# Kernel optimization log

Measured on AMD Instinct MI355X. Metric: run time of the kernel, lower is better.

The kernel has to match this reference:

```python
import jax, jax.numpy as jnp
import numpy as np

B, S, D, DFF = 4, 2048, 1024, 4096
EPS = 1e-5


def layernorm(x, gamma, beta):
    mu = jnp.mean(x, axis=-1, keepdims=True)
    var = jnp.var(x, axis=-1, keepdims=True)
    return (x - mu) * jax.lax.rsqrt(var + EPS) * gamma + beta


def attention(Q, K, V, causal):
    d_k = Q.shape[-1]
    scores = jnp.einsum('bqd,bkd->bqk', Q, K) / jnp.sqrt(jnp.asarray(d_k, Q.dtype))
    if causal:
        q_len, k_len = scores.shape[-2], scores.shape[-1]
        mask = jnp.tril(jnp.ones((q_len, k_len), dtype=bool))
        scores = jnp.where(mask[None], scores, jnp.asarray(-jnp.inf, scores.dtype))
    w = jax.nn.softmax(scores, axis=-1)
    return jnp.einsum('bqk,bkd->bqd', w, V)


def setup_inputs() -> dict:
    key = jax.random.key(0)
    ks = jax.random.split(key, 12)
    sd = 0.02
    return {
        'y': jax.random.normal(ks[0], (B, S, D), jnp.float32),
        'Z': jax.random.normal(ks[1], (B, S, D), jnp.float32),
        'w1': jax.random.normal(ks[2], (D, DFF), jnp.float32) * sd,
        'b1': jnp.zeros((DFF,), jnp.float32),
        'w2': jax.random.normal(ks[3], (DFF, D), jnp.float32) * sd,
        'b2': jnp.zeros((D,), jnp.float32),
        'g1': jnp.ones((D,), jnp.float32), 'beta1': jnp.zeros((D,), jnp.float32),
        'g2': jnp.ones((D,), jnp.float32), 'beta2': jnp.zeros((D,), jnp.float32),
        'g3': jnp.ones((D,), jnp.float32), 'beta3': jnp.zeros((D,), jnp.float32),
    }


def reference(y, Z, w1, b1, w2, b2, g1, beta1, g2, beta2, g3, beta3):
    # masked (causal) self-attention, single head over full d_model
    sa = attention(y, y, y, causal=True)
    y = layernorm(y + sa, g1, beta1)
    # cross-attention to encoder memory Z
    ca = attention(y, Z, Z, causal=False)
    y = layernorm(y + ca, g2, beta2)
    # position-wise FFN
    h = jax.nn.relu(jnp.einsum('bsd,df->bsf', y, w1) + b1)
    ff = jnp.einsum('bsf,fd->bsd', h, w2) + b2
    y = layernorm(y + ff, g3, beta3)
    return y
```

## Files before the change

kernel.cpp:

```cpp
#include <hip/hip_runtime.h>
#include <hip/hip_bf16.h>


#define Bb 4
#define Ss 2048
#define Dd 1024
#define Ff 4096

typedef __attribute__((ext_vector_type(4))) float f32x4;
typedef __attribute__((ext_vector_type(8))) short bf16x8;
typedef __attribute__((ext_vector_type(8))) unsigned short u16x8;
typedef __attribute__((ext_vector_type(4))) unsigned short u16x4;

__device__ __forceinline__ unsigned short f2bf(float f) {
  unsigned u = __float_as_uint(f);
  u += 0x7FFFu + ((u >> 16) & 1u);
  return (unsigned short)(u >> 16);
}
__device__ __forceinline__ float bf2f(unsigned short h) {
  return __uint_as_float(((unsigned)h) << 16);
}

__device__ __forceinline__ void gload_lds16(const void* g, void* l) {
  __builtin_amdgcn_global_load_lds((const __attribute__((address_space(1))) void*)g,
                                   (__attribute__((address_space(3))) void*)l, 16, 0, 0);
}

__device__ __forceinline__ int xcd8(int orig, int n) {
  int q = n >> 3, r = n & 7;
  int x = orig & 7;
  int base = x < r ? x * (q + 1) : r * (q + 1) + (x - r) * q;
  return base + (orig >> 3);
}

__global__ __launch_bounds__(256) void k_transpose_cast(const float* __restrict__ in,
                                                        unsigned short* __restrict__ outT,
                                                        unsigned short* __restrict__ outR,
                                                        int R, int C) {
  __shared__ float t[32][33];
  size_t bo = (size_t)blockIdx.z * R * C;
  const float* pin = in + bo;
  unsigned short* poutT = outT + bo;
  unsigned short* poutR = outR ? outR + bo : nullptr;
  int c0 = blockIdx.x * 32, r0 = blockIdx.y * 32;
  int tx = threadIdx.x, ty = threadIdx.y;
#pragma unroll
  for (int i = 0; i < 4; i++) {
    float v = pin[(size_t)(r0 + ty + i * 8) * C + c0 + tx];
    t[ty + i * 8][tx] = v;
    if (poutR) poutR[(size_t)(r0 + ty + i * 8) * C + c0 + tx] = f2bf(v);
  }
  __syncthreads();
#pragma unroll
  for (int i = 0; i < 4; i++)
    poutT[(size_t)(c0 + ty + i * 8) * R + r0 + tx] = f2bf(t[tx][ty + i * 8]);
}

#define BAR() __builtin_amdgcn_s_barrier()
#define PRIO1() __builtin_amdgcn_s_setprio(1)
#define PRIO0() __builtin_amdgcn_s_setprio(0)

#define LDA8(arr, mh, bo)                                                       \
  {                                                                             \
    _Pragma("unroll") for (int j_ = 0; j_ < QM; ++j_) {                         \
      _Pragma("unroll") for (int kh_ = 0; kh_ < 2; ++kh_) {                     \
        arr[j_][kh_] =                                                          \
            *(const bf16x8*)(lds + (bo) + ((mh)*QM + j_) * 2048 + aof[kh_]);    \
      }                                                                         \
    }                                                                           \
  }

#define LDB8(arr, nh, bo)                                                       \
  {                                                                             \
    _Pragma("unroll") for (int n_ = 0; n_ < 2; ++n_) {                          \
      _Pragma("unroll") for (int kh_ = 0; kh_ < 2; ++kh_) {                     \
        arr[n_][kh_] =                                                          \
            *(const bf16x8*)(lds + (bo) + ((nh)*2 + n_) * 2048 + bof[kh_]);     \
      }                                                                         \
    }                                                                           \
  }

#define MMQ(aarr, barr, mh, nh)                                                 \
  {                                                                             \
    _Pragma("unroll") for (int j_ = 0; j_ < QM; ++j_) {                         \
      _Pragma("unroll") for (int n_ = 0; n_ < 2; ++n_) {                        \
        _Pragma("unroll") for (int kh_ = 0; kh_ < 2; ++kh_) {                   \
          acc[(mh)*QM + j_][(nh)*2 + n_] = __builtin_amdgcn_mfma_f32_16x16x32_bf16( \
              aarr[j_][kh_], barr[n_][kh_], acc[(mh)*QM + j_][(nh)*2 + n_], 0, 0, 0); \
        }                                                                       \
      }                                                                         \
    }                                                                           \
  }

#define EPILOGUE(MR_, WMS_)                                                     \
  {                                                                             \
    const int colb = j0 + wc * 64 + fr;                                         \
    const int rowb = i0 + wr * (WMS_) + (kq << 2);                              \
    const size_t cb = (size_t)bz * bsC;                                         \
    _Pragma("unroll") for (int m = 0; m < (MR_); ++m) {                         \
      _Pragma("unroll") for (int r = 0; r < 4; ++r) {                           \
        size_t ro = cb + (size_t)(rowb + m * 16 + r) * ldc;                     \
        _Pragma("unroll") for (int n = 0; n < 4; ++n) {                         \
          float v = acc[m][n][r];                                               \
          int col = colb + n * 16;                                              \
          if (EPI == 0) Cb[ro + col] = f2bf(v * scale);                         \
          else if (EPI == 2) Cb[ro + col] = f2bf(fmaxf(v + bias[col], 0.f));    \
          else if (EPI == 4) Cb[ro + col] = f2bf(v + resid[ro + col]);          \
          else Cb[ro + col] = f2bf(v + bias[col] + resid[ro + col]);            \
        }                                                                       \
      }                                                                         \
    }                                                                           \
  }

template <int EPI, bool CAUSAL>
__global__ __launch_bounds__(512) void k_gemm8(
    const unsigned short* __restrict__ Ag, const unsigned short* __restrict__ Bg,
    unsigned short* __restrict__ Cb,
    const float* __restrict__ bias, const float* __restrict__ resid,
    int K, int lda, int ldb, int ldc, long bsA, long bsB, long bsC, float scale) {
  constexpr int QM = 4;
  constexpr int ABYTES = 32768, BBYTES = 32768;
  __shared__ alignas(16) char lds[2 * ABYTES + 2 * BBYTES];

  int i0, j0;
  if (CAUSAL) {
    int t = xcd8(blockIdx.x, gridDim.x);
    int ti = (int)((sqrtf(8.f * t + 1.f) - 1.f) * 0.5f);
    while ((ti + 1) * (ti + 2) / 2 <= t) ++ti;
    while (ti * (ti + 1) / 2 > t) --ti;
    i0 = ti * 256;
    j0 = (t - ti * (ti + 1) / 2) * 256;
  } else {
    int lin = xcd8(blockIdx.y * gridDim.x + blockIdx.x, gridDim.x * gridDim.y);
    i0 = (lin / gridDim.x) * 256;
    j0 = (lin % gridDim.x) * 256;
  }
  int bz = blockIdx.z;
  Ag += (size_t)bz * bsA;
  Bg += (size_t)bz * bsB;

  const int nk = K / 64;
  const int niter = nk / 2;

  const int tid = threadIdx.x;
  const int w = tid >> 6, lane = tid & 63;
  const int wr = w >> 2, wc = w & 3;

  const int srow = (w << 3) + (lane >> 3);
  const int bcs = (lane & 7) ^ (lane >> 3);
  const unsigned short* As = Ag + (size_t)(i0 + srow) * lda + bcs * 8;
  const unsigned short* Bs = Bg + (size_t)(j0 + srow) * ldb + bcs * 8;
  char* ldsAw = lds + w * 1024;
  char* ldsBw = lds + 2 * ABYTES + w * 1024;

  auto stA = [&](int kt, int hf) {
    int ks = kt < nk ? kt : nk - 1;
#pragma unroll
    for (int l = 0; l < 2; ++l)
      gload_lds16(As + (size_t)(hf * 128 + l * 64) * lda + ks * 64,
                  ldsAw + (kt & 1) * ABYTES + hf * 128 * 128 + l * 8192);
  };
  auto stB = [&](int kt, int hf) {
    int ks = kt < nk ? kt : nk - 1;
#pragma unroll
    for (int l = 0; l < 2; ++l)
      gload_lds16(Bs + (size_t)(hf * 128 + l * 64) * ldb + ks * 64,
                  ldsBw + (kt & 1) * BBYTES + hf * 128 * 128 + l * 8192);
  };

  const int fr = lane & 15, kq = lane >> 4;
  const int rA = wr * 128 + fr;
  const int rB = wc * 64 + fr;
  unsigned aof[2], bof[2];
  aof[0] = rA * 128 + ((kq ^ (rA & 7)) << 4);
  aof[1] = rA * 128 + (((kq + 4) ^ (rA & 7)) << 4);
  bof[0] = 2 * ABYTES + rB * 128 + ((kq ^ (rB & 7)) << 4);
  bof[1] = 2 * ABYTES + rB * 128 + (((kq + 4) ^ (rB & 7)) << 4);
  constexpr int A0 = 0, A1 = ABYTES, B0 = 0, B1 = BBYTES;

  f32x4 acc[8][4];
#pragma unroll
  for (int m = 0; m < 8; ++m)
#pragma unroll
    for (int n = 0; n < 4; ++n) acc[m][n] = (f32x4){0.f, 0.f, 0.f, 0.f};

  bf16x8 a0[QM][2], a1[QM][2], b0[2][2], b1[2][2];

  stA(0, 0); stA(0, 1); stB(0, 0); stB(0, 1);
  stA(1, 0); stA(1, 1); stB(1, 0);
  asm volatile("s_waitcnt vmcnt(6)" ::: "memory");
  BAR();
  LDA8(a0, 0, A0); LDB8(b0, 0, B0);

  for (int t = 0; t < niter; ++t) {
    const int ka = 2 * t + 2, kb = 2 * t + 3;
    LDA8(a1, 1, A0);
    stB(2 * t + 1, 1);
    BAR(); PRIO1(); MMQ(a0, b0, 0, 0); PRIO0(); BAR();
    LDB8(b1, 1, B0);
    stA(ka, 0);
    BAR(); PRIO1(); MMQ(a1, b0, 1, 0); PRIO0(); BAR();
    stA(ka, 1);
    BAR(); PRIO1(); MMQ(a0, b1, 0, 1); PRIO0(); BAR();
    stB(ka, 0);
    asm volatile("s_waitcnt vmcnt(6)" ::: "memory");
    BAR();
    LDA8(a0, 0, A1); LDB8(b0, 0, B1);
    PRIO1(); MMQ(a1, b1, 1, 1); PRIO0(); BAR();
    LDA8(a1, 1, A1);
    stB(ka, 1);
    BAR(); PRIO1(); MMQ(a0, b0, 0, 0); PRIO0(); BAR();
    LDB8(b1, 1, B1);
    stA(kb, 0);
    BAR(); PRIO1(); MMQ(a1, b0, 1, 0); PRIO0(); BAR();
    stA(kb, 1);
    BAR(); PRIO1(); MMQ(a0, b1, 0, 1); PRIO0(); BAR();
    stB(kb, 0);
    asm volatile("s_waitcnt vmcnt(6)" ::: "memory");
    BAR();
    LDA8(a0, 0, A0); LDB8(b0, 0, B0);
    PRIO1(); MMQ(a1, b1, 1, 1); PRIO0(); BAR();
  }
  EPILOGUE(8, 128)
}

template <int EPI, bool KCAP>
__global__ __launch_bounds__(512) void k_gemm4(
    const unsigned short* __restrict__ Ag, const unsigned short* __restrict__ Bg,
    unsigned short* __restrict__ Cb,
    const float* __restrict__ bias, const float* __restrict__ resid,
    int K, int lda, int ldb, int ldc, long bsA, long bsB, long bsC, float scale) {
  constexpr int QM = 4;
  constexpr int ABYTES = 16384, BBYTES = 32768;
  __shared__ alignas(16) char lds[2 * ABYTES + 2 * BBYTES];

  int lin = xcd8(blockIdx.y * gridDim.x + blockIdx.x, gridDim.x * gridDim.y);
  int i0 = (lin / gridDim.x) * 128;
  int j0 = (lin % gridDim.x) * 256;
  int bz = blockIdx.z;
  Ag += (size_t)bz * bsA;
  Bg += (size_t)bz * bsB;

  int nk = K / 64;
  if (KCAP) {
    int cap = i0 / 64 + 2;
    nk = nk < cap ? nk : cap;
  }
  const int niter = nk / 2;

  const int tid = threadIdx.x;
  const int w = tid >> 6, lane = tid & 63;
  const int wr = w >> 2, wc = w & 3;

  const int srow = (w << 3) + (lane >> 3);
  const int bcs = (lane & 7) ^ (lane >> 3);
  const unsigned short* As = Ag + (size_t)(i0 + srow) * lda + bcs * 8;
  const unsigned short* Bs = Bg + (size_t)(j0 + srow) * ldb + bcs * 8;
  char* ldsAw = lds + w * 1024;
  char* ldsBw = lds + 2 * ABYTES + w * 1024;

  auto stA2 = [&](int kt) {
    int ks = kt < nk ? kt : nk - 1;
#pragma unroll
    for (int hf = 0; hf < 2; ++hf)
      gload_lds16(As + (size_t)(hf * 64) * lda + ks * 64,
                  ldsAw + (kt & 1) * ABYTES + hf * 64 * 128);
  };
  auto stBh = [&](int kt, int hf) {
    int ks = kt < nk ? kt : nk - 1;
#pragma unroll
    for (int l = 0; l < 2; ++l)
      gload_lds16(Bs + (size_t)(hf * 128 + l * 64) * ldb + ks * 64,
                  ldsBw + (kt & 1) * BBYTES + hf * 128 * 128 + l * 8192);
  };

  const int fr = lane & 15, kq = lane >> 4;
  const int rA = wr * 64 + fr;
  const int rB = wc * 64 + fr;
  unsigned aof[2], bof[2];
  aof[0] = rA * 128 + ((kq ^ (rA & 7)) << 4);
  aof[1] = rA * 128 + (((kq + 4) ^ (rA & 7)) << 4);
  bof[0] = 2 * ABYTES + rB * 128 + ((kq ^ (rB & 7)) << 4);
  bof[1] = 2 * ABYTES + rB * 128 + (((kq + 4) ^ (rB & 7)) << 4);
  constexpr int A0 = 0, A1 = ABYTES, B0 = 0, B1 = BBYTES;

  f32x4 acc[4][4];
#pragma unroll
  for (int m = 0; m < 4; ++m)
#pragma unroll
    for (int n = 0; n < 4; ++n) acc[m][n] = (f32x4){0.f, 0.f, 0.f, 0.f};

  bf16x8 a[QM][2], b0[2][2], b1[2][2];

  stA2(0); stBh(0, 0); stBh(0, 1);
  stA2(1); stBh(1, 0);
  asm volatile("s_waitcnt vmcnt(4)" ::: "memory");
  BAR();
  LDA8(a, 0, A0); LDB8(b0, 0, B0);

  for (int t = 0; t < niter; ++t) {
    const int ka = 2 * t + 2, kb = 2 * t + 3;
    LDB8(b1, 1, B0);
    stBh(2 * t + 1, 1);
    BAR(); PRIO1(); MMQ(a, b0, 0, 0); PRIO0(); BAR();
    stA2(ka); stBh(ka, 0);
    asm volatile("s_waitcnt vmcnt(4)" ::: "memory");
    BAR();
    PRIO1(); MMQ(a, b1, 0, 1); PRIO0();
    LDA8(a, 0, A1); LDB8(b0, 0, B1);
    BAR();
    LDB8(b1, 1, B1);
    stBh(ka, 1);
    BAR(); PRIO1(); MMQ(a, b0, 0, 0); PRIO0(); BAR();
    stA2(kb); stBh(kb, 0);
    asm volatile("s_waitcnt vmcnt(4)" ::: "memory");
    BAR();
    PRIO1(); MMQ(a, b1, 0, 1); PRIO0();
    LDA8(a, 0, A0); LDB8(b0, 0, B0);
    BAR();
  }
  EPILOGUE(4, 64)
}

template <bool CAUSAL>
__global__ __launch_bounds__(256) void k_softmax(unsigned short* __restrict__ scores) {
  int row = blockIdx.x;
  int i = row & (Ss - 1);
  unsigned short* src = scores + (size_t)row * Ss;
  int nv = CAUSAL ? i + 1 : Ss;
  int nb = CAUSAL ? ((i & ~127) + 128) : Ss;
  int t = threadIdx.x;
  int w = t >> 6, lane = t & 63;
  bool act = t * 8 < nb;
  float v[8];
  float mx = -1e30f;
  if (act) {
    u16x8 raw = *(const u16x8*)(src + t * 8);
#pragma unroll
    for (int k = 0; k < 8; k++) {
      int j = t * 8 + k;
      v[k] = (j < nv) ? bf2f(raw[k]) : -1e30f;
      mx = fmaxf(mx, v[k]);
    }
  } else {
#pragma unroll
    for (int k = 0; k < 8; k++) v[k] = -1e30f;
  }
#pragma unroll
  for (int o = 32; o; o >>= 1) mx = fmaxf(mx, __shfl_xor(mx, o));
  __shared__ float red[8];
  if (lane == 0) red[w] = mx;
  __syncthreads();
  mx = fmaxf(fmaxf(red[0], red[1]), fmaxf(red[2], red[3]));
  float sum = 0.f;
#pragma unroll
  for (int k = 0; k < 8; k++) {
    float e = (v[k] > -1e29f) ? __expf(v[k] - mx) : 0.f;
    v[k] = e;
    sum += e;
  }
#pragma unroll
  for (int o = 32; o; o >>= 1) sum += __shfl_xor(sum, o);
  if (lane == 0) red[4 + w] = sum;
  __syncthreads();
  sum = red[4] + red[5] + red[6] + red[7];
  float inv = 1.f / sum;
  if (act) {
    u16x8 r;
#pragma unroll
    for (int k = 0; k < 8; k++) r[k] = f2bf(v[k] * inv);
    *(u16x8*)(src + t * 8) = r;
  }
}

__global__ __launch_bounds__(256) void k_ln(const unsigned short* __restrict__ a,
                                            const float* __restrict__ g,
                                            const float* __restrict__ be,
                                            float* __restrict__ outf,
                                            unsigned short* __restrict__ outb) {
  int row = blockIdx.x;
  size_t o = (size_t)row * Dd;
  int t = threadIdx.x;
  u16x4 raw = *(const u16x4*)(a + o + t * 4);
  f32x4 x;
#pragma unroll
  for (int k = 0; k < 4; k++) x[k] = bf2f(raw[k]);
  float s = x[0] + x[1] + x[2] + x[3];
  float q = x[0] * x[0] + x[1] * x[1] + x[2] * x[2] + x[3] * x[3];
  int w = t >> 6, lane = t & 63;
#pragma unroll
  for (int of = 32; of; of >>= 1) {
    s += __shfl_xor(s, of);
    q += __shfl_xor(q, of);
  }
  __shared__ float red[8];
  if (lane == 0) {
    red[w] = s;
    red[4 + w] = q;
  }
  __syncthreads();
  s = red[0] + red[1] + red[2] + red[3];
  q = red[4] + red[5] + red[6] + red[7];
  float mean = s * (1.f / Dd);
  float var = q * (1.f / Dd) - mean * mean;
  float rstd = rsqrtf(var + 1e-5f);
  f32x4 gv = *(const f32x4*)(g + t * 4);
  f32x4 bv = *(const f32x4*)(be + t * 4);
  f32x4 y;
#pragma unroll
  for (int k = 0; k < 4; k++) y[k] = (x[k] - mean) * rstd * gv[k] + bv[k];
  *(f32x4*)(outf + o + t * 4) = y;
  if (outb) {
    u16x4 r;
    r[0] = f2bf(y[0]); r[1] = f2bf(y[1]); r[2] = f2bf(y[2]); r[3] = f2bf(y[3]);
    *(u16x4*)(outb + o + t * 4) = r;
  }
}

extern "C" void kernel_launch(void* const* d_in, const int* in_sizes, int n_in, void* d_out,
                              int out_size, void* d_ws, size_t ws_size, hipStream_t stream) {
  (void)in_sizes; (void)n_in; (void)out_size; (void)ws_size;
  const float* y   = (const float*)d_in[0];
  const float* Z   = (const float*)d_in[1];
  const float* w1  = (const float*)d_in[2];
  const float* b1  = (const float*)d_in[3];
  const float* w2  = (const float*)d_in[4];
  const float* b2  = (const float*)d_in[5];
  const float* g1  = (const float*)d_in[6];
  const float* be1 = (const float*)d_in[7];
  const float* g2  = (const float*)d_in[8];
  const float* be2 = (const float*)d_in[9];
  const float* g3  = (const float*)d_in[10];
  const float* be3 = (const float*)d_in[11];
  float* out = (float*)d_out;

  char* ws = (char*)d_ws;
  const size_t MB = 1024ull * 1024ull;
  unsigned short* T   = (unsigned short*)(ws);
  unsigned short* Zbf = (unsigned short*)(ws + 16 * MB);
  unsigned short* ybf = (unsigned short*)(ws + 32 * MB);
  unsigned short* w1t = (unsigned short*)(ws + 48 * MB);
  unsigned short* w2t = (unsigned short*)(ws + 56 * MB);
  unsigned short* sc  = (unsigned short*)(ws + 64 * MB);
  unsigned short* h   = (unsigned short*)(ws + 64 * MB);
  unsigned short* Zt  = (unsigned short*)(ws + 96 * MB);
  float* res          = (float*)(ws + 128 * MB);
  unsigned short* attnb = (unsigned short*)d_out;

  dim3 b256(256), b512(512);
  const float scl = 1.f / 32.f;
  const long SD = (long)Ss * Dd, SS = (long)Ss * Ss;

  k_transpose_cast<<<dim3(Dd / 32, Ss / 32, Bb), dim3(32, 8), 0, stream>>>(y, T, ybf, Ss, Dd);
  k_transpose_cast<<<dim3(Dd / 32, Ss / 32, Bb), dim3(32, 8), 0, stream>>>(Z, Zt, Zbf, Ss, Dd);
  k_transpose_cast<<<dim3(Ff / 32, Dd / 32, 1), dim3(32, 8), 0, stream>>>(w1, w1t, nullptr, Dd, Ff);
  k_transpose_cast<<<dim3(Dd / 32, Ff / 32, 1), dim3(32, 8), 0, stream>>>(w2, w2t, nullptr, Ff, Dd);

  k_gemm8<0, true><<<dim3(36, 1, Bb), b512, 0, stream>>>(
      ybf, ybf, sc, nullptr, nullptr, Dd, Dd, Dd, Ss, SD, SD, SS, scl);
  k_softmax<true><<<dim3(Bb * Ss), b256, 0, stream>>>(sc);
  k_gemm4<4, true><<<dim3(Dd / 256, Ss / 128, Bb), b512, 0, stream>>>(
      sc, T, attnb, nullptr, y, Ss, Ss, Ss, Dd, SS, SD, SD, 1.f);
  k_ln<<<dim3(Bb * Ss), b256, 0, stream>>>(attnb, g1, be1, res, ybf);

  k_gemm8<0, false><<<dim3(Ss / 256, Ss / 256, Bb), b512, 0, stream>>>(
      ybf, Zbf, sc, nullptr, nullptr, Dd, Dd, Dd, Ss, SD, SD, SS, scl);
  k_softmax<false><<<dim3(Bb * Ss), b256, 0, stream>>>(sc);
  k_gemm4<4, false><<<dim3(Dd / 256, Ss / 128, Bb), b512, 0, stream>>>(
      sc, Zt, attnb, nullptr, res, Ss, Ss, Ss, Dd, SS, SD, SD, 1.f);
  k_ln<<<dim3(Bb * Ss), b256, 0, stream>>>(attnb, g2, be2, res, ybf);

  k_gemm8<2, false><<<dim3(Ff / 256, (Bb * Ss) / 256, 1), b512, 0, stream>>>(
      ybf, w1t, h, b1, nullptr, Dd, Dd, Dd, Ff, 0L, 0L, 0L, 1.f);
  k_gemm4<5, false><<<dim3(Dd / 256, (Bb * Ss) / 128, 1), b512, 0, stream>>>(
      h, w2t, T, b2, res, Ff, Ff, Ff, Dd, 0L, 0L, 0L, 1.f);
  k_ln<<<dim3(Bb * Ss), b256, 0, stream>>>(T, g3, be3, out, nullptr);
}
```

Measured before the change: 376.3 us.

## Compute attention score GEMMs in FP8 e4m3 with permuted-column layout

The two QK^T score GEMMs (causal self-attention and cross-attention) now run on FP8 e4m3 MFMA instead of bf16. Their inputs (y, Z and the first LayerNorm output) are emitted as FP8 with a per-64-byte column permutation so the new kernel's LDS reads line up with the fp8 MFMA operand layout. This halves the input bytes and LDS footprint for those GEMMs and uses the faster fp8 matrix instructions. The cost is reduced precision in the attention scores: unnormalized inputs of magnitude up to about 4 with K=1024 could push softmax errors past tolerance.

```diff
diff --git a/kernel.cpp b/kernel.cpp
--- a/kernel.cpp
+++ b/kernel.cpp
@@ -1,5 +1,6 @@
 #include <hip/hip_runtime.h>
 #include <hip/hip_bf16.h>
+#include <hip/hip_fp8.h>
 
 
 #define Bb 4
@@ -9,6 +10,7 @@
 
 typedef __attribute__((ext_vector_type(4))) float f32x4;
 typedef __attribute__((ext_vector_type(8))) short bf16x8;
+typedef __attribute__((ext_vector_type(2))) long i64x2;
 typedef __attribute__((ext_vector_type(8))) unsigned short u16x8;
 typedef __attribute__((ext_vector_type(4))) unsigned short u16x4;
 
@@ -19,6 +21,14 @@
 }
 __device__ __forceinline__ float bf2f(unsigned short h) {
   return __uint_as_float(((unsigned)h) << 16);
+}
+__device__ __forceinline__ unsigned char f2f8(float f) {
+  __hip_fp8_e4m3 q(f);
+  return q.__x;
+}
+__device__ __forceinline__ int f8col(int c) {
+  int g = c >> 6, b = c & 63, o = b >> 3, j = b & 7;
+  return g * 64 + (2 * (o & 3) + (o >> 2)) * 8 + j;
 }
 
 __device__ __forceinline__ void gload_lds16(const void* g, void* l) {
@@ -35,20 +45,20 @@
 
 __global__ __launch_bounds__(256) void k_transpose_cast(const float* __restrict__ in,
                                                         unsigned short* __restrict__ outT,
-                                                        unsigned short* __restrict__ outR,
+                                                        unsigned char* __restrict__ out8,
                                                         int R, int C) {
   __shared__ float t[32][33];
   size_t bo = (size_t)blockIdx.z * R * C;
   const float* pin = in + bo;
   unsigned short* poutT = outT + bo;
-  unsigned short* poutR = outR ? outR + bo : nullptr;
+  unsigned char* pout8 = out8 ? out8 + bo : nullptr;
   int c0 = blockIdx.x * 32, r0 = blockIdx.y * 32;
   int tx = threadIdx.x, ty = threadIdx.y;
 #pragma unroll
   for (int i = 0; i < 4; i++) {
     float v = pin[(size_t)(r0 + ty + i * 8) * C + c0 + tx];
     t[ty + i * 8][tx] = v;
-    if (poutR) poutR[(size_t)(r0 + ty + i * 8) * C + c0 + tx] = f2bf(v);
+    if (pout8) pout8[(size_t)(r0 + ty + i * 8) * C + f8col(c0 + tx)] = f2f8(v);
   }
   __syncthreads();
 #pragma unroll
@@ -87,6 +97,28 @@
         _Pragma("unroll") for (int kh_ = 0; kh_ < 2; ++kh_) {                   \
           acc[(mh)*QM + j_][(nh)*2 + n_] = __builtin_amdgcn_mfma_f32_16x16x32_bf16( \
               aarr[j_][kh_], barr[n_][kh_], acc[(mh)*QM + j_][(nh)*2 + n_], 0, 0, 0); \
+        }                                                                       \
+      }                                                                         \
+    }                                                                           \
+  }
+
+#define LDAF8(arr, mh, bo)                                                      \
+  {                                                                             \
+    _Pragma("unroll") for (int j_ = 0; j_ < 4; ++j_)                            \
+        arr[j_] = *(const i64x2*)(lds + (bo) + ((mh)*4 + j_) * 1024 + aofs);    \
+  }
+#define LDBF8(arr, nh, bo)                                                      \
+  {                                                                             \
+    _Pragma("unroll") for (int n_ = 0; n_ < 2; ++n_)                            \
+        arr[n_] = *(const i64x2*)(lds + (bo) + ((nh)*2 + n_) * 1024 + bofs);    \
+  }
+#define MMQF8(aarr, barr, mh, nh)                                               \
+  {                                                                             \
+    _Pragma("unroll") for (int j_ = 0; j_ < 4; ++j_) {                          \
+      _Pragma("unroll") for (int n_ = 0; n_ < 2; ++n_) {                        \
+        _Pragma("unroll") for (int kh_ = 0; kh_ < 2; ++kh_) {                   \
+          acc[(mh)*4 + j_][(nh)*2 + n_] = __builtin_amdgcn_mfma_f32_16x16x32_fp8_fp8( \
+              aarr[j_][kh_], barr[n_][kh_], acc[(mh)*4 + j_][(nh)*2 + n_], 0, 0, 0);  \
         }                                                                       \
       }                                                                         \
     }                                                                           \
@@ -112,6 +144,120 @@
     }                                                                           \
   }
 
+template <bool CAUSAL>
+__global__ __launch_bounds__(512) void k_gemm8f8(
+    const unsigned char* __restrict__ Ag, const unsigned char* __restrict__ Bg,
+    unsigned short* __restrict__ Cb,
+    int K, int lda, int ldb, int ldc, long bsA, long bsB, long bsC, float scale) {
+  constexpr int ABYTES = 16384, BBYTES = 16384;
+  __shared__ alignas(16) char lds[2 * ABYTES + 2 * BBYTES];
+
+  int i0, j0;
+  if (CAUSAL) {
+    int t = xcd8(blockIdx.x, gridDim.x);
+    int ti = (int)((sqrtf(8.f * t + 1.f) - 1.f) * 0.5f);
+    while ((ti + 1) * (ti + 2) / 2 <= t) ++ti;
+    while (ti * (ti + 1) / 2 > t) --ti;
+    i0 = ti * 256;
+    j0 = (t - ti * (ti + 1) / 2) * 256;
+  } else {
+    int lin = xcd8(blockIdx.y * gridDim.x + blockIdx.x, gridDim.x * gridDim.y);
+    i0 = (lin / gridDim.x) * 256;
+    j0 = (lin % gridDim.x) * 256;
+  }
+  int bz = blockIdx.z;
+  Ag += (size_t)bz * bsA;
+  Bg += (size_t)bz * bsB;
+
+  const int nk = K / 64;
+  const int niter = nk / 2;
+
+  const int tid = threadIdx.x;
+  const int w = tid >> 6, lane = tid & 63;
+  const int wr = w >> 2, wc = w & 3;
+
+  const int srow = tid >> 2;
+  const int scs = (tid & 3) ^ ((tid >> 3) & 3);
+  const unsigned char* As = Ag + (size_t)(i0 + srow) * lda + scs * 16;
+  const unsigned char* Bs = Bg + (size_t)(j0 + srow) * ldb + scs * 16;
+
+  auto stA = [&](int kt, int hf) {
+    int ks = kt < nk ? kt : nk - 1;
+    gload_lds16(As + (size_t)(hf * 128) * lda + ks * 64,
+                lds + (kt & 1) * ABYTES + hf * 8192 + w * 1024);
+  };
+  auto stB = [&](int kt, int hf) {
+    int ks = kt < nk ? kt : nk - 1;
+    gload_lds16(Bs + (size_t)(hf * 128) * ldb + ks * 64,
+                lds + 2 * ABYTES + (kt & 1) * BBYTES + hf * 8192 + w * 1024);
+  };
+
+  const int fr = lane & 15, kq = lane >> 4;
+  const int rA = wr * 128 + fr;
+  const int rB = wc * 64 + fr;
+  const unsigned aofs = rA * 64 + ((kq ^ ((rA >> 1) & 3)) << 4);
+  const unsigned bofs = rB * 64 + ((kq ^ ((rB >> 1) & 3)) << 4);
+  constexpr int A0 = 0, A1 = ABYTES, B0 = 2 * ABYTES, B1 = 2 * ABYTES + BBYTES;
+
+  f32x4 acc[8][4];
+#pragma unroll
+  for (int m = 0; m < 8; ++m)
+#pragma unroll
+    for (int n = 0; n < 4; ++n) acc[m][n] = (f32x4){0.f, 0.f, 0.f, 0.f};
+
+  i64x2 a0[4], a1[4], b0[2], b1[2];
+
+  stA(0, 0); stA(0, 1); stB(0, 0); stB(0, 1);
+  stA(1, 0); stA(1, 1); stB(1, 0);
+  asm volatile("s_waitcnt vmcnt(3)" ::: "memory");
+  BAR();
+  LDAF8(a0, 0, A0); LDBF8(b0, 0, B0);
+
+  for (int t = 0; t < niter; ++t) {
+    const int ka = 2 * t + 2, kb = 2 * t + 3;
+    LDAF8(a1, 1, A0);
+    stB(2 * t + 1, 1);
+    BAR(); PRIO1(); MMQF8(a0, b0, 0, 0); PRIO0(); BAR();
+    LDBF8(b1, 1, B0);
+    stA(ka, 0);
+    BAR(); PRIO1(); MMQF8(a1, b0, 1, 0); PRIO0(); BAR();
+    stA(ka, 1);
+    BAR(); PRIO1(); MMQF8(a0, b1, 0, 1); PRIO0(); BAR();
+    stB(ka, 0);
+    asm volatile("s_waitcnt vmcnt(3)" ::: "memory");
+    BAR();
+    LDAF8(a0, 0, A1); LDBF8(b0, 0, B1);
+    PRIO1(); MMQF8(a1, b1, 1, 1); PRIO0(); BAR();
+    LDAF8(a1, 1, A1);
+    stB(ka, 1);
+    BAR(); PRIO1(); MMQF8(a0, b0, 0, 0); PRIO0(); BAR();
+    LDBF8(b1, 1, B1);
+    stA(kb, 0);
+    BAR(); PRIO1(); MMQF8(a1, b0, 1, 0); PRIO0(); BAR();
+    stA(kb, 1);
+    BAR(); PRIO1(); MMQF8(a0, b1, 0, 1); PRIO0(); BAR();
+    stB(kb, 0);
+    asm volatile("s_waitcnt vmcnt(3)" ::: "memory");
+    BAR();
+    LDAF8(a0, 0, A0); LDBF8(b0, 0, B0);
+    PRIO1(); MMQF8(a1, b1, 1, 1); PRIO0(); BAR();
+  }
+
+  const int colb = j0 + wc * 64 + fr;
+  const int rowb = i0 + wr * 128 + (kq << 2);
+  const size_t cb = (size_t)bz * bsC;
+#pragma unroll
+  for (int m = 0; m < 8; ++m) {
+#pragma unroll
+    for (int r = 0; r < 4; ++r) {
+      size_t ro = cb + (size_t)(rowb + m * 16 + r) * ldc;
+#pragma unroll
+      for (int n = 0; n < 4; ++n)
+        Cb[ro + colb + n * 16] = f2bf(acc[m][n][r] * scale);
+    }
+  }
+}
+
 template <int EPI, bool CAUSAL>
 __global__ __launch_bounds__(512) void k_gemm8(
     const unsigned short* __restrict__ Ag, const unsigned short* __restrict__ Bg,
@@ -373,11 +519,13 @@
   }
 }
 
+template <int OM>
 __global__ __launch_bounds__(256) void k_ln(const unsigned short* __restrict__ a,
                                             const float* __restrict__ g,
                                             const float* __restrict__ be,
                                             float* __restrict__ outf,
-                                            unsigned short* __restrict__ outb) {
+                                            unsigned short* __restrict__ outb,
+                                            unsigned char* __restrict__ out8) {
   int row = blockIdx.x;
   size_t o = (size_t)row * Dd;
   int t = threadIdx.x;
@@ -410,10 +558,17 @@
 #pragma unroll
   for (int k = 0; k < 4; k++) y[k] = (x[k] - mean) * rstd * gv[k] + bv[k];
   *(f32x4*)(outf + o + t * 4) = y;
-  if (outb) {
+  if (OM == 1) {
     u16x4 r;
     r[0] = f2bf(y[0]); r[1] = f2bf(y[1]); r[2] = f2bf(y[2]); r[3] = f2bf(y[3]);
     *(u16x4*)(outb + o + t * 4) = r;
+  } else if (OM == 2) {
+    int cbyte = t * 4;
+    int gq = cbyte >> 6, oo = (cbyte >> 3) & 7, j = cbyte & 7;
+    int phys = gq * 64 + (2 * (oo & 3) + (oo >> 2)) * 8 + j;
+    unsigned r = (unsigned)f2f8(y[0]) | ((unsigned)f2f8(y[1]) << 8) |
+                 ((unsigned)f2f8(y[2]) << 16) | ((unsigned)f2f8(y[3]) << 24);
+    *(unsigned*)(out8 + (size_t)row * Dd + phys) = r;
   }
 }
 
@@ -437,13 +592,15 @@
   char* ws = (char*)d_ws;
   const size_t MB = 1024ull * 1024ull;
   unsigned short* T   = (unsigned short*)(ws);
-  unsigned short* Zbf = (unsigned short*)(ws + 16 * MB);
+  unsigned short* Zt  = (unsigned short*)(ws + 16 * MB);
   unsigned short* ybf = (unsigned short*)(ws + 32 * MB);
   unsigned short* w1t = (unsigned short*)(ws + 48 * MB);
   unsigned short* w2t = (unsigned short*)(ws + 56 * MB);
   unsigned short* sc  = (unsigned short*)(ws + 64 * MB);
   unsigned short* h   = (unsigned short*)(ws + 64 * MB);
-  unsigned short* Zt  = (unsigned short*)(ws + 96 * MB);
+  unsigned char* y8   = (unsigned char*)(ws + 96 * MB);
+  unsigned char* Z8   = (unsigned char*)(ws + 104 * MB);
+  unsigned char* y18  = (unsigned char*)(ws + 112 * MB);
   float* res          = (float*)(ws + 128 * MB);
   unsigned short* attnb = (unsigned short*)d_out;
 
@@ -451,28 +608,28 @@
   const float scl = 1.f / 32.f;
   const long SD = (long)Ss * Dd, SS = (long)Ss * Ss;
 
-  k_transpose_cast<<<dim3(Dd / 32, Ss / 32, Bb), dim3(32, 8), 0, stream>>>(y, T, ybf, Ss, Dd);
-  k_transpose_cast<<<dim3(Dd / 32, Ss / 32, Bb), dim3(32, 8), 0, stream>>>(Z, Zt, Zbf, Ss, Dd);
+  k_transpose_cast<<<dim3(Dd / 32, Ss / 32, Bb), dim3(32, 8), 0, stream>>>(y, T, y8, Ss, Dd);
+  k_transpose_cast<<<dim3(Dd / 32, Ss / 32, Bb), dim3(32, 8), 0, stream>>>(Z, Zt, Z8, Ss, Dd);
   k_transpose_cast<<<dim3(Ff / 32, Dd / 32, 1), dim3(32, 8), 0, stream>>>(w1, w1t, nullptr, Dd, Ff);
   k_transpose_cast<<<dim3(Dd / 32, Ff / 32, 1), dim3(32, 8), 0, stream>>>(w2, w2t, nullptr, Ff, Dd);
 
-  k_gemm8<0, true><<<dim3(36, 1, Bb), b512, 0, stream>>>(
-      ybf, ybf, sc, nullptr, nullptr, Dd, Dd, Dd, Ss, SD, SD, SS, scl);
+  k_gemm8f8<true><<<dim3(36, 1, Bb), b512, 0, stream>>>(
+      y8, y8, sc, Dd, Dd, Dd, Ss, SD, SD, SS, scl);
   k_softmax<true><<<dim3(Bb * Ss), b256, 0, stream>>>(sc);
   k_gemm4<4, true><<<dim3(Dd / 256, Ss / 128, Bb), b512, 0, stream>>>(
       sc, T, attnb, nullptr, y, Ss, Ss, Ss, Dd, SS, SD, SD, 1.f);
-  k_ln<<<dim3(Bb * Ss), b256, 0, stream>>>(attnb, g1, be1, res, ybf);
-
-  k_gemm8<0, false><<<dim3(Ss / 256, Ss / 256, Bb), b512, 0, stream>>>(
-      ybf, Zbf, sc, nullptr, nullptr, Dd, Dd, Dd, Ss, SD, SD, SS, scl);
+  k_ln<2><<<dim3(Bb * Ss), b256, 0, stream>>>(attnb, g1, be1, res, nullptr, y18);
+
+  k_gemm8f8<false><<<dim3(Ss / 256, Ss / 256, Bb), b512, 0, stream>>>(
+      y18, Z8, sc, Dd, Dd, Dd, Ss, SD, SD, SS, scl);
   k_softmax<false><<<dim3(Bb * Ss), b256, 0, stream>>>(sc);
   k_gemm4<4, false><<<dim3(Dd / 256, Ss / 128, Bb), b512, 0, stream>>>(
       sc, Zt, attnb, nullptr, res, Ss, Ss, Ss, Dd, SS, SD, SD, 1.f);
-  k_ln<<<dim3(Bb * Ss), b256, 0, stream>>>(attnb, g2, be2, res, ybf);
+  k_ln<1><<<dim3(Bb * Ss), b256, 0, stream>>>(attnb, g2, be2, res, ybf, nullptr);
 
   k_gemm8<2, false><<<dim3(Ff / 256, (Bb * Ss) / 256, 1), b512, 0, stream>>>(
       ybf, w1t, h, b1, nullptr, Dd, Dd, Dd, Ff, 0L, 0L, 0L, 1.f);
   k_gemm4<5, false><<<dim3(Dd / 256, (Bb * Ss) / 128, 1), b512, 0, stream>>>(
       h, w2t, T, b2, res, Ff, Ff, Ff, Dd, 0L, 0L, 0L, 1.f);
-  k_ln<<<dim3(Bb * Ss), b256, 0, stream>>>(T, g3, be3, out, nullptr);
-}
+  k_ln<0><<<dim3(Bb * Ss), b256, 0, stream>>>(T, g3, be3, out, nullptr, nullptr);
+}
```

Measured after the change: 367.1 us. 1.03x faster.
